# Optimization experiments

Measured on AMD Instinct MI355X. Metric: run time of the kernel, lower is better.

The kernel has to match this reference:

```python
import jax, jax.numpy as jnp
import numpy as np

NUM_CLASSES = 1000
FEAT_DIM = 512
BATCH = 65536


def setup_inputs() -> dict:
    key = jax.random.key(0)
    k1, k2, k3 = jax.random.split(key, 3)
    features = jax.random.normal(k1, (BATCH, FEAT_DIM), dtype=jnp.float32)
    centers = jax.random.normal(k2, (NUM_CLASSES, FEAT_DIM), dtype=jnp.float32)
    labels = jax.random.randint(k3, (BATCH,), 0, NUM_CLASSES, dtype=jnp.int64)
    return {"features": features, "centers": centers, "labels": labels}


def reference(features, centers, labels):
    # Torch loop: for each class j with count>0, add F.mse_loss(z_j, center_j)
    # = sum_{i: l_i=j} ||f_i - c_j||^2 / (count_j * feat_dim); final /= batch_size.
    batch_size, feat_dim = features.shape
    num_classes = centers.shape[0]
    labels = labels.astype(jnp.int32)
    c = jax.lax.stop_gradient(centers)  # centers are detached in the original
    # per-sample squared distance to its own class center: [batch]
    diff = features - c[labels]
    d = jnp.sum(diff * diff, axis=-1)
    # per-class sums and counts in one segment-reduce pass
    sums = jax.ops.segment_sum(d, labels, num_segments=num_classes)
    counts = jax.ops.segment_sum(jnp.ones_like(d), labels, num_segments=num_classes)
    per_class = jnp.where(counts > 0, sums / (counts * feat_dim), 0.0)
    return jnp.sum(per_class) / batch_size
```

## Files before the change

### kernel.cpp

```cpp
#include <hip/hip_runtime.h>


#define WAVE 64

__global__ __launch_bounds__(256) void center_dist_kernel(
    const float* __restrict__ features,
    const float* __restrict__ centers,
    const int*   __restrict__ labels,
    float* __restrict__ sums,
    float* __restrict__ counts,
    int batch, int feat)
{
    const int wave_in_block = threadIdx.x >> 6;
    const int lane          = threadIdx.x & 63;
    const int sample        = blockIdx.x * 4 + wave_in_block;
    if (sample >= batch) return;

    const int label = labels[sample];

    const float4* __restrict__ f4 =
        (const float4*)(features + (size_t)sample * feat);
    const float4* __restrict__ c4 =
        (const float4*)(centers + (size_t)label * feat);

    float acc = 0.0f;
    const int n4 = feat >> 2;
#pragma unroll 2
    for (int idx = lane; idx < n4; idx += WAVE) {
        float4 fv = f4[idx];
        float4 cv = c4[idx];
        float dx = fv.x - cv.x;
        float dy = fv.y - cv.y;
        float dz = fv.z - cv.z;
        float dw = fv.w - cv.w;
        acc += dx * dx + dy * dy;
        acc += dz * dz + dw * dw;
    }

#pragma unroll
    for (int off = 32; off > 0; off >>= 1)
        acc += __shfl_down(acc, off, WAVE);

    if (lane == 0) {
        atomicAdd(&sums[label], acc);
        atomicAdd(&counts[label], 1.0f);
    }
}

__global__ __launch_bounds__(256) void center_finalize_kernel(
    const float* __restrict__ sums,
    const float* __restrict__ counts,
    float* __restrict__ out,
    int nclass, int feat, int batch)
{
    float acc = 0.0f;
    for (int j = threadIdx.x; j < nclass; j += blockDim.x) {
        float n = counts[j];
        if (n > 0.0f) acc += sums[j] / (n * (float)feat);
    }
#pragma unroll
    for (int off = 32; off > 0; off >>= 1)
        acc += __shfl_down(acc, off, WAVE);

    __shared__ float warp_part[4];
    const int lane = threadIdx.x & 63;
    const int wid  = threadIdx.x >> 6;
    if (lane == 0) warp_part[wid] = acc;
    __syncthreads();

    if (threadIdx.x == 0) {
        float total = warp_part[0] + warp_part[1] + warp_part[2] + warp_part[3];
        out[0] = total / (float)batch;
    }
}

extern "C" void kernel_launch(void* const* d_in, const int* in_sizes, int n_in,
                              void* d_out, int out_size, void* d_ws, size_t ws_size,
                              hipStream_t stream) {
    const float* features = (const float*)d_in[0];
    const float* centers  = (const float*)d_in[1];
    const int*   labels   = (const int*)d_in[2];

    const int batch  = in_sizes[2];
    const int feat   = in_sizes[0] / batch;
    const int nclass = in_sizes[1] / feat;

    float* sums   = (float*)d_ws;
    float* counts = sums + nclass;

    hipMemsetAsync(d_ws, 0, (size_t)2 * nclass * sizeof(float), stream);

    const int blocks = (batch + 3) / 4;
    center_dist_kernel<<<blocks, 256, 0, stream>>>(
        features, centers, labels, sums, counts, batch, feat);

    center_finalize_kernel<<<1, 256, 0, stream>>>(
        sums, counts, (float*)d_out, nclass, feat, batch);
}
```

Baseline: 191.9 us.

## Precompute class counts and replace float atomics with per-block partial reduction

Adds a separate int-atomic counting pass over labels, then scales each sample's squared distance by its class count inside the distance kernel. Per-block partial sums then go through a final single-block reduction. This removes the per-sample float atomicAdd pairs on the class sums and counts arrays, and each wave now handles several samples. The cost is an extra kernel launch and a second read of the labels, and the summation order differs from the per-class grouping.

```diff
diff --git a/kernel.cpp b/kernel.cpp
--- a/kernel.cpp
+++ b/kernel.cpp
@@ -2,76 +2,85 @@
 
 
 #define WAVE 64
+constexpr int WAVES_PER_BLOCK  = 4;
+constexpr int SAMPLES_PER_WAVE = 4;
+constexpr int SAMPLES_PER_BLOCK = WAVES_PER_BLOCK * SAMPLES_PER_WAVE;
 
-__global__ __launch_bounds__(256) void center_dist_kernel(
+__global__ __launch_bounds__(256) void count_kernel(
+    const int* __restrict__ labels, int* __restrict__ counts, int batch)
+{
+    int i = blockIdx.x * blockDim.x + threadIdx.x;
+    if (i < batch) atomicAdd(&counts[labels[i]], 1);
+}
+
+__global__ __launch_bounds__(256) void dist_kernel(
     const float* __restrict__ features,
     const float* __restrict__ centers,
     const int*   __restrict__ labels,
-    float* __restrict__ sums,
-    float* __restrict__ counts,
+    const int*   __restrict__ counts,
+    float* __restrict__ partials,
     int batch, int feat)
 {
-    const int wave_in_block = threadIdx.x >> 6;
-    const int lane          = threadIdx.x & 63;
-    const int sample        = blockIdx.x * 4 + wave_in_block;
-    if (sample >= batch) return;
+    const int wid  = threadIdx.x >> 6;
+    const int lane = threadIdx.x & 63;
+    const int base = blockIdx.x * SAMPLES_PER_BLOCK + wid * SAMPLES_PER_WAVE;
+    const int n4   = feat >> 2;
 
-    const int label = labels[sample];
+    float local = 0.0f;
+#pragma unroll
+    for (int s = 0; s < SAMPLES_PER_WAVE; ++s) {
+        const int sample = base + s;
+        if (sample >= batch) break;
+        const int label = labels[sample];
 
-    const float4* __restrict__ f4 =
-        (const float4*)(features + (size_t)sample * feat);
-    const float4* __restrict__ c4 =
-        (const float4*)(centers + (size_t)label * feat);
+        const float4* __restrict__ f4 =
+            (const float4*)(features + (size_t)sample * feat);
+        const float4* __restrict__ c4 =
+            (const float4*)(centers + (size_t)label * feat);
 
+        float acc = 0.0f;
+#pragma unroll 2
+        for (int idx = lane; idx < n4; idx += WAVE) {
+            float4 fv = f4[idx];
+            float4 cv = c4[idx];
+            float dx = fv.x - cv.x;
+            float dy = fv.y - cv.y;
+            float dz = fv.z - cv.z;
+            float dw = fv.w - cv.w;
+            acc += dx * dx + dy * dy + dz * dz + dw * dw;
+        }
+        local += acc / ((float)counts[label] * (float)feat);
+    }
+
+#pragma unroll
+    for (int off = 32; off > 0; off >>= 1)
+        local += __shfl_down(local, off, WAVE);
+
+    __shared__ float wpart[WAVES_PER_BLOCK];
+    if (lane == 0) wpart[wid] = local;
+    __syncthreads();
+    if (threadIdx.x == 0)
+        partials[blockIdx.x] = wpart[0] + wpart[1] + wpart[2] + wpart[3];
+}
+
+__global__ __launch_bounds__(256) void reduce_kernel(
+    const float* __restrict__ partials, int n,
+    float* __restrict__ out, int batch)
+{
     float acc = 0.0f;
-    const int n4 = feat >> 2;
-#pragma unroll 2
-    for (int idx = lane; idx < n4; idx += WAVE) {
-        float4 fv = f4[idx];
-        float4 cv = c4[idx];
-        float dx = fv.x - cv.x;
-        float dy = fv.y - cv.y;
-        float dz = fv.z - cv.z;
-        float dw = fv.w - cv.w;
-        acc += dx * dx + dy * dy;
-        acc += dz * dz + dw * dw;
-    }
+    for (int i = threadIdx.x; i < n; i += 256) acc += partials[i];
 
 #pragma unroll
     for (int off = 32; off > 0; off >>= 1)
         acc += __shfl_down(acc, off, WAVE);
 
-    if (lane == 0) {
-        atomicAdd(&sums[label], acc);
-        atomicAdd(&counts[label], 1.0f);
-    }
-}
-
-__global__ __launch_bounds__(256) void center_finalize_kernel(
-    const float* __restrict__ sums,
-    const float* __restrict__ counts,
-    float* __restrict__ out,
-    int nclass, int feat, int batch)
-{
-    float acc = 0.0f;
-    for (int j = threadIdx.x; j < nclass; j += blockDim.x) {
-        float n = counts[j];
-        if (n > 0.0f) acc += sums[j] / (n * (float)feat);
-    }
-#pragma unroll
-    for (int off = 32; off > 0; off >>= 1)
-        acc += __shfl_down(acc, off, WAVE);
-
-    __shared__ float warp_part[4];
+    __shared__ float wpart[4];
     const int lane = threadIdx.x & 63;
     const int wid  = threadIdx.x >> 6;
-    if (lane == 0) warp_part[wid] = acc;
+    if (lane == 0) wpart[wid] = acc;
     __syncthreads();
-
-    if (threadIdx.x == 0) {
-        float total = warp_part[0] + warp_part[1] + warp_part[2] + warp_part[3];
-        out[0] = total / (float)batch;
-    }
+    if (threadIdx.x == 0)
+        out[0] = (wpart[0] + wpart[1] + wpart[2] + wpart[3]) / (float)batch;
 }
 
 extern "C" void kernel_launch(void* const* d_in, const int* in_sizes, int n_in,
@@ -85,15 +94,16 @@
     const int feat   = in_sizes[0] / batch;
     const int nclass = in_sizes[1] / feat;
 
-    float* sums   = (float*)d_ws;
-    float* counts = sums + nclass;
+    int*   counts   = (int*)d_ws;
+    float* partials = (float*)((char*)d_ws + ((nclass * sizeof(int) + 255) & ~255));
 
-    hipMemsetAsync(d_ws, 0, (size_t)2 * nclass * sizeof(float), stream);
+    hipMemsetAsync(counts, 0, (size_t)nclass * sizeof(int), stream);
 
-    const int blocks = (batch + 3) / 4;
-    center_dist_kernel<<<blocks, 256, 0, stream>>>(
-        features, centers, labels, sums, counts, batch, feat);
+    count_kernel<<<(batch + 255) / 256, 256, 0, stream>>>(labels, counts, batch);
 
-    center_finalize_kernel<<<1, 256, 0, stream>>>(
-        sums, counts, (float*)d_out, nclass, feat, batch);
+    const int nblocks = (batch + SAMPLES_PER_BLOCK - 1) / SAMPLES_PER_BLOCK;
+    dist_kernel<<<nblocks, 256, 0, stream>>>(
+        features, centers, labels, counts, partials, batch, feat);
+
+    reduce_kernel<<<1, 256, 0, stream>>>(partials, nblocks, (float*)d_out, batch);
 }
```

After: 213.7 us. +11.3%, slower.

## Fuse memset, distance and finalize into one cooperative persistent kernel

Applied to the files above, without the earlier changes.

Replaces the memset, the per-sample distance kernel and the single-block finalize with one cooperative kernel using grid syncs. Counts are computed first with integer atomics, so each sample's distance can be divided by its class count inline. Each block then needs only one float atomic, instead of two atomics per sample. This removes launch overhead and per-sample atomic contention but adds three grid-wide barriers and a grid-stride loop over samples on a fixed 1024-block grid.

```diff
diff --git a/kernel.cpp b/kernel.cpp
--- a/kernel.cpp
+++ b/kernel.cpp
@@ -1,77 +1,79 @@
 #include <hip/hip_runtime.h>
+#include <hip/hip_cooperative_groups.h>
+
+namespace cg = cooperative_groups;
 
 
 #define WAVE 64
+constexpr int THREADS = 256;
+constexpr int BLOCKS  = 1024;
 
-__global__ __launch_bounds__(256) void center_dist_kernel(
+__global__ __launch_bounds__(THREADS) void centerloss_fused(
     const float* __restrict__ features,
     const float* __restrict__ centers,
     const int*   __restrict__ labels,
-    float* __restrict__ sums,
-    float* __restrict__ counts,
-    int batch, int feat)
+    int*   __restrict__ counts,
+    float* __restrict__ accum,
+    float* __restrict__ out,
+    int batch, int feat, int nclass)
 {
-    const int wave_in_block = threadIdx.x >> 6;
-    const int lane          = threadIdx.x & 63;
-    const int sample        = blockIdx.x * 4 + wave_in_block;
-    if (sample >= batch) return;
+    cg::grid_group grid = cg::this_grid();
+    const int tid      = blockIdx.x * blockDim.x + threadIdx.x;
+    const int nthreads = gridDim.x * blockDim.x;
 
-    const int label = labels[sample];
+    for (int j = tid; j < nclass; j += nthreads) counts[j] = 0;
+    if (tid == 0) *accum = 0.0f;
+    grid.sync();
 
-    const float4* __restrict__ f4 =
-        (const float4*)(features + (size_t)sample * feat);
-    const float4* __restrict__ c4 =
-        (const float4*)(centers + (size_t)label * feat);
+    for (int i = tid; i < batch; i += nthreads)
+        atomicAdd(&counts[labels[i]], 1);
+    grid.sync();
 
-    float acc = 0.0f;
-    const int n4 = feat >> 2;
+    const int wave_id = tid >> 6;
+    const int lane    = tid & 63;
+    const int nwaves  = nthreads >> 6;
+    const int n4      = feat >> 2;
+
+    float local = 0.0f;
+    for (int sample = wave_id; sample < batch; sample += nwaves) {
+        const int label = labels[sample];
+        const float4* __restrict__ f4 =
+            (const float4*)(features + (size_t)sample * feat);
+        const float4* __restrict__ c4 =
+            (const float4*)(centers + (size_t)label * feat);
+
+        float acc = 0.0f;
 #pragma unroll 2
-    for (int idx = lane; idx < n4; idx += WAVE) {
-        float4 fv = f4[idx];
-        float4 cv = c4[idx];
-        float dx = fv.x - cv.x;
-        float dy = fv.y - cv.y;
-        float dz = fv.z - cv.z;
-        float dw = fv.w - cv.w;
-        acc += dx * dx + dy * dy;
-        acc += dz * dz + dw * dw;
+        for (int idx = lane; idx < n4; idx += WAVE) {
+            float4 fv = f4[idx];
+            float4 cv = c4[idx];
+            float dx = fv.x - cv.x;
+            float dy = fv.y - cv.y;
+            float dz = fv.z - cv.z;
+            float dw = fv.w - cv.w;
+            acc += dx * dx + dy * dy + dz * dz + dw * dw;
+        }
+        local += acc / (float)counts[label];
     }
+    local *= 1.0f / (float)feat;
 
 #pragma unroll
     for (int off = 32; off > 0; off >>= 1)
-        acc += __shfl_down(acc, off, WAVE);
+        local += __shfl_down(local, off, WAVE);
 
-    if (lane == 0) {
-        atomicAdd(&sums[label], acc);
-        atomicAdd(&counts[label], 1.0f);
+    __shared__ float wpart[THREADS / WAVE];
+    const int wib = threadIdx.x >> 6;
+    if (lane == 0) wpart[wib] = local;
+    __syncthreads();
+    if (threadIdx.x == 0) {
+        float b = 0.0f;
+#pragma unroll
+        for (int w = 0; w < THREADS / WAVE; ++w) b += wpart[w];
+        atomicAdd(accum, b);
     }
-}
+    grid.sync();
 
-__global__ __launch_bounds__(256) void center_finalize_kernel(
-    const float* __restrict__ sums,
-    const float* __restrict__ counts,
-    float* __restrict__ out,
-    int nclass, int feat, int batch)
-{
-    float acc = 0.0f;
-    for (int j = threadIdx.x; j < nclass; j += blockDim.x) {
-        float n = counts[j];
-        if (n > 0.0f) acc += sums[j] / (n * (float)feat);
-    }
-#pragma unroll
-    for (int off = 32; off > 0; off >>= 1)
-        acc += __shfl_down(acc, off, WAVE);
-
-    __shared__ float warp_part[4];
-    const int lane = threadIdx.x & 63;
-    const int wid  = threadIdx.x >> 6;
-    if (lane == 0) warp_part[wid] = acc;
-    __syncthreads();
-
-    if (threadIdx.x == 0) {
-        float total = warp_part[0] + warp_part[1] + warp_part[2] + warp_part[3];
-        out[0] = total / (float)batch;
-    }
+    if (tid == 0) out[0] = *accum / (float)batch;
 }
 
 extern "C" void kernel_launch(void* const* d_in, const int* in_sizes, int n_in,
@@ -80,20 +82,22 @@
     const float* features = (const float*)d_in[0];
     const float* centers  = (const float*)d_in[1];
     const int*   labels   = (const int*)d_in[2];
+    float*       out      = (float*)d_out;
 
-    const int batch  = in_sizes[2];
-    const int feat   = in_sizes[0] / batch;
-    const int nclass = in_sizes[1] / feat;
+    int batch  = in_sizes[2];
+    int feat   = in_sizes[0] / batch;
+    int nclass = in_sizes[1] / feat;
 
-    float* sums   = (float*)d_ws;
-    float* counts = sums + nclass;
+    int*   counts = (int*)d_ws;
+    float* accum  = (float*)((char*)d_ws + ((nclass * sizeof(int) + 255) & ~255));
 
-    hipMemsetAsync(d_ws, 0, (size_t)2 * nclass * sizeof(float), stream);
+    void* args[] = {
+        (void*)&features, (void*)&centers, (void*)&labels,
+        (void*)&counts, (void*)&accum, (void*)&out,
+        (void*)&batch, (void*)&feat, (void*)&nclass
+    };
 
-    const int blocks = (batch + 3) / 4;
-    center_dist_kernel<<<blocks, 256, 0, stream>>>(
-        features, centers, labels, sums, counts, batch, feat);
-
-    center_finalize_kernel<<<1, 256, 0, stream>>>(
-        sums, counts, (float*)d_out, nclass, feat, batch);
+    hipLaunchCooperativeKernel((const void*)centerloss_fused,
+                               dim3(BLOCKS), dim3(THREADS),
+                               args, 0, stream);
 }
```

Measured after the change: 467.9 us. 144% more time.

## Fuse distance and finalize kernels via last-block ticket with grid-stride loop

Applied to the files above, without the earlier changes.

Merges the per-sample distance kernel and the single-block finalize kernel into one launch. A fixed grid of 2048 blocks walks the samples with a grid-stride loop, and the last block to arrive, found through an atomic ticket counter, does the per-class reduction. This removes one kernel launch and the gap between the two kernels. In exchange it adds a threadfence, an atomic ticket per block and a serial tail in the last block.

```diff
diff --git a/kernel.cpp b/kernel.cpp
--- a/kernel.cpp
+++ b/kernel.cpp
@@ -2,75 +2,85 @@
 
 
 #define WAVE 64
+constexpr int THREADS = 256;
+constexpr int WAVES_PER_BLOCK = THREADS / WAVE;
+constexpr int NBLOCKS = 2048;
 
-__global__ __launch_bounds__(256) void center_dist_kernel(
+__global__ __launch_bounds__(THREADS) void centerloss_kernel(
     const float* __restrict__ features,
     const float* __restrict__ centers,
     const int*   __restrict__ labels,
     float* __restrict__ sums,
     float* __restrict__ counts,
-    int batch, int feat)
+    unsigned* __restrict__ ticket,
+    float* __restrict__ out,
+    int batch, int feat, int nclass)
 {
-    const int wave_in_block = threadIdx.x >> 6;
-    const int lane          = threadIdx.x & 63;
-    const int sample        = blockIdx.x * 4 + wave_in_block;
-    if (sample >= batch) return;
+    const int wib    = threadIdx.x >> 6;
+    const int lane   = threadIdx.x & 63;
+    const int gwave  = blockIdx.x * WAVES_PER_BLOCK + wib;
+    const int nwaves = gridDim.x * WAVES_PER_BLOCK;
+    const int n4     = feat >> 2;
 
-    const int label = labels[sample];
+    for (int sample = gwave; sample < batch; sample += nwaves) {
+        const int label = labels[sample];
+        const float4* __restrict__ f4 =
+            (const float4*)(features + (size_t)sample * feat);
+        const float4* __restrict__ c4 =
+            (const float4*)(centers + (size_t)label * feat);
 
-    const float4* __restrict__ f4 =
-        (const float4*)(features + (size_t)sample * feat);
-    const float4* __restrict__ c4 =
-        (const float4*)(centers + (size_t)label * feat);
+        float acc = 0.0f;
+#pragma unroll 2
+        for (int idx = lane; idx < n4; idx += WAVE) {
+            float4 fv = f4[idx];
+            float4 cv = c4[idx];
+            float dx = fv.x - cv.x;
+            float dy = fv.y - cv.y;
+            float dz = fv.z - cv.z;
+            float dw = fv.w - cv.w;
+            acc += dx * dx + dy * dy + dz * dz + dw * dw;
+        }
+#pragma unroll
+        for (int off = 32; off > 0; off >>= 1)
+            acc += __shfl_down(acc, off, WAVE);
 
-    float acc = 0.0f;
-    const int n4 = feat >> 2;
-#pragma unroll 2
-    for (int idx = lane; idx < n4; idx += WAVE) {
-        float4 fv = f4[idx];
-        float4 cv = c4[idx];
-        float dx = fv.x - cv.x;
-        float dy = fv.y - cv.y;
-        float dz = fv.z - cv.z;
-        float dw = fv.w - cv.w;
-        acc += dx * dx + dy * dy;
-        acc += dz * dz + dw * dw;
+        if (lane == 0) {
+            atomicAdd(&sums[label], acc);
+            atomicAdd(&counts[label], 1.0f);
+        }
     }
 
-#pragma unroll
-    for (int off = 32; off > 0; off >>= 1)
-        acc += __shfl_down(acc, off, WAVE);
+    __threadfence();
+    __syncthreads();
+    __shared__ int is_last;
+    if (threadIdx.x == 0) {
+        unsigned old = atomicAdd(ticket, 1u);
+        is_last = (old == (unsigned)(gridDim.x - 1));
+    }
+    __syncthreads();
+    if (!is_last) return;
 
-    if (lane == 0) {
-        atomicAdd(&sums[label], acc);
-        atomicAdd(&counts[label], 1.0f);
-    }
-}
-
-__global__ __launch_bounds__(256) void center_finalize_kernel(
-    const float* __restrict__ sums,
-    const float* __restrict__ counts,
-    float* __restrict__ out,
-    int nclass, int feat, int batch)
-{
-    float acc = 0.0f;
-    for (int j = threadIdx.x; j < nclass; j += blockDim.x) {
-        float n = counts[j];
-        if (n > 0.0f) acc += sums[j] / (n * (float)feat);
+    __threadfence();
+    float total = 0.0f;
+    for (int j = threadIdx.x; j < nclass; j += THREADS) {
+        float n = __hip_atomic_load(&counts[j], __ATOMIC_RELAXED,
+                                    __HIP_MEMORY_SCOPE_AGENT);
+        float s = __hip_atomic_load(&sums[j], __ATOMIC_RELAXED,
+                                    __HIP_MEMORY_SCOPE_AGENT);
+        if (n > 0.5f) total += s / n;
     }
 #pragma unroll
     for (int off = 32; off > 0; off >>= 1)
-        acc += __shfl_down(acc, off, WAVE);
+        total += __shfl_down(total, off, WAVE);
 
-    __shared__ float warp_part[4];
-    const int lane = threadIdx.x & 63;
-    const int wid  = threadIdx.x >> 6;
-    if (lane == 0) warp_part[wid] = acc;
+    __shared__ float wpart[WAVES_PER_BLOCK];
+    if (lane == 0) wpart[wib] = total;
     __syncthreads();
-
     if (threadIdx.x == 0) {
-        float total = warp_part[0] + warp_part[1] + warp_part[2] + warp_part[3];
-        out[0] = total / (float)batch;
+        float t = 0.0f;
+#pragma unroll
+        for (int w = 0; w < WAVES_PER_BLOCK; ++w) t += wpart[w];
+        out[0] = t / ((float)feat * (float)batch);
     }
 }
 
@@ -85,15 +95,13 @@
     const int feat   = in_sizes[0] / batch;
     const int nclass = in_sizes[1] / feat;
 
-    float* sums   = (float*)d_ws;
-    float* counts = sums + nclass;
+    float*    sums   = (float*)d_ws;
+    float*    counts = sums + nclass;
+    unsigned* ticket = (unsigned*)(counts + nclass);
 
-    hipMemsetAsync(d_ws, 0, (size_t)2 * nclass * sizeof(float), stream);
+    hipMemsetAsync(d_ws, 0, (size_t)(2 * nclass + 1) * sizeof(float), stream);
 
-    const int blocks = (batch + 3) / 4;
-    center_dist_kernel<<<blocks, 256, 0, stream>>>(
-        features, centers, labels, sums, counts, batch, feat);
-
-    center_finalize_kernel<<<1, 256, 0, stream>>>(
-        sums, counts, (float*)d_out, nclass, feat, batch);
+    centerloss_kernel<<<NBLOCKS, THREADS, 0, stream>>>(
+        features, centers, labels, sums, counts, ticket,
+        (float*)d_out, batch, feat, nclass);
 }
```

Measured after the change: 513.8 us. +167.7%, slower.
